# Performance work log

Measured on AMD Instinct MI355X. Metric: run time of the kernel, lower is better.

Reference implementation:

```python
import jax, jax.numpy as jnp
import numpy as np
import math


def _alibi_slopes(h):
    # h must be a power of 2 here (h=16); matches pow2slopes in the source
    start = 2.0 ** (-2.0 ** (-(math.log2(h) - 3.0)))
    return jnp.asarray([start ** (i + 1) for i in range(h)], dtype=jnp.float32)


def setup_inputs() -> dict:
    key = jax.random.key(0)
    ks = jax.random.split(key, 7)
    B, N, d, h, r = 2, 2048, 1024, 16, 32
    dk = d // h
    x = jax.random.normal(ks[0], (B, N, d), dtype=jnp.float32)
    # causal additive mask (standard usage of the optional `mask` arg)
    i = jnp.arange(N)[:, None]
    j = jnp.arange(N)[None, :]
    mask = jnp.where(j > i, jnp.float32(-1e9), jnp.float32(0.0))[None, None]  # [1,1,N,N]
    s = 1.0 / math.sqrt(d)
    Wq = jax.random.normal(ks[1], (d, d), dtype=jnp.float32) * s
    Wk = jax.random.normal(ks[2], (d, d), dtype=jnp.float32) * s
    Wv = jax.random.normal(ks[3], (d, d), dtype=jnp.float32) * s
    # orthogonal init of U, as in nn.init.orthogonal_
    U, _ = jnp.linalg.qr(jax.random.normal(ks[4], (dk, r), dtype=jnp.float32))
    Wproj = jax.random.normal(ks[5], (d, h * r), dtype=jnp.float32) * (1.0 / math.sqrt(h * r))
    return {"x": x, "mask": mask, "Wq": Wq, "Wk": Wk, "Wv": Wv, "U": U,
            "Wproj": Wproj, "rel_bias_tokens": N}


def reference(x, mask, Wq, Wk, Wv, U, Wproj, rel_bias_tokens):
    B, N, d = x.shape
    dk, r = U.shape
    h = d // dk

    def lowrank_proj(W):
        # Linear(d,d,bias=False) then per-head low-rank projection by U
        y = (x @ W.T).reshape(B, N, h, dk)          # [B,N,h,dk]
        return jnp.einsum('bnhk,kr->bhnr', y, U)     # [B,h,N,r]

    q = lowrank_proj(Wq)
    k = lowrank_proj(Wk)
    v = lowrank_proj(Wv)

    # scores scaled by sqrt(dk) (NOT sqrt(r)) -- faithful to source
    att = jnp.einsum('bhnr,bhmr->bhnm', q, k) / math.sqrt(dk)  # [B,h,N,N]

    # q_len == k_len branch: alibi bias + mask
    i = jnp.arange(rel_bias_tokens)[:, None]
    j = jnp.arange(rel_bias_tokens)[None, :]
    dist = jnp.maximum(j - i, 0).astype(att.dtype)             # clamp_min(0)
    slopes = _alibi_slopes(h)
    att = att + (-slopes[:, None, None] * dist)[None] + mask

    z = jnp.einsum('bhnm,bhmr->bhnr', jax.nn.softmax(att, axis=-1), v)
    z = z.transpose(0, 2, 1, 3).reshape(B, N, h * r)
    # dropout is identity in eval
    return z @ Wproj.T
```

## Files before the change

kernel.cpp:

```cpp
#include <hip/hip_runtime.h>
#include <hip/hip_bf16.h>
#include <stdint.h>

typedef unsigned short u16;
typedef __attribute__((ext_vector_type(4))) short short4v;
typedef __attribute__((ext_vector_type(8))) short short8;
typedef __attribute__((ext_vector_type(4))) float f32x4;

#define NB 2
#define NN 2048
#define ND 1024
#define NH 16
#define NR 32
#define NM (NB*NN)
#define NHR 512
#define NQKV 1536

static __device__ __forceinline__ u16 f2bf(float f) {
  union { float f; uint32_t u; } v; v.f = f;
  uint32_t r = v.u + 0x7fffu + ((v.u >> 16) & 1u);
  return (u16)(r >> 16);
}
static __device__ __forceinline__ u16 fastbf(float f) {
  union { float f; uint32_t u; } v; v.f = f;
  return (u16)((v.u + 0x8000u) >> 16);
}

typedef __attribute__((address_space(1))) unsigned int as1_u32;
typedef __attribute__((address_space(3))) unsigned int as3_u32;

static __device__ __forceinline__ void async_copy16(void* lds, const void* g) {
  __builtin_amdgcn_global_load_lds((as1_u32*)(uintptr_t)g,
                                   (as3_u32*)(uint32_t)(uintptr_t)lds,
                                   16, 0, 0);
}

__global__ void cast_f32_bf16(const float* __restrict__ in, u16* __restrict__ o,
                              int n8) {
  int i = blockIdx.x * 256 + threadIdx.x;
  if (i >= n8) return;
  const float4* p = (const float4*)in + (size_t)i * 2;
  float4 a = p[0], b = p[1];
  short8 v;
  v[0] = f2bf(a.x); v[1] = f2bf(a.y); v[2] = f2bf(a.z); v[3] = f2bf(a.w);
  v[4] = f2bf(b.x); v[5] = f2bf(b.y); v[6] = f2bf(b.z); v[7] = f2bf(b.w);
  *((short8*)o + i) = v;
}

__global__ __launch_bounds__(256, 2)
void build_wct(const float* __restrict__ Wq, const float* __restrict__ Wk,
               const float* __restrict__ Wv, const float* __restrict__ U,
               u16* __restrict__ WcT) {
  __shared__ float sU[64 * 32];
  const int tid = threadIdx.x;
  #pragma unroll
  for (int t = 0; t < 2; ++t)
    ((float4*)sU)[t * 256 + tid] = ((const float4*)U)[t * 256 + tid];
  __syncthreads();
  const int wh = blockIdx.y;
  const int w = wh >> 4, head = wh & 15;
  const float* W = (w == 0) ? Wq : (w == 1 ? Wk : Wv);
  const int i = blockIdx.x * 256 + tid;
  const float* Wcol = W + (size_t)head * 64 * ND + i;
  float acc[32];
  #pragma unroll
  for (int rr = 0; rr < 32; ++rr) acc[rr] = 0.f;
  for (int kk = 0; kk < 64; ++kk) {
    const float wv = Wcol[(size_t)kk * ND];
    const float4* u4 = (const float4*)&sU[kk * 32];
    #pragma unroll
    for (int r4 = 0; r4 < 8; ++r4) {
      float4 u = u4[r4];
      acc[r4 * 4 + 0] += wv * u.x;
      acc[r4 * 4 + 1] += wv * u.y;
      acc[r4 * 4 + 2] += wv * u.z;
      acc[r4 * 4 + 3] += wv * u.w;
    }
  }
  const float sc = (w == 0) ? 0.125f : 1.0f;
  const int colBase = w * 512 + head * 32;
  #pragma unroll
  for (int rr = 0; rr < 32; ++rr)
    WcT[(size_t)(colBase + rr) * ND + i] = f2bf(acc[rr] * sc);
}

template<int EPI>
__global__ __launch_bounds__(256, 2)
void gemm_bt(const u16* __restrict__ A, int lda,
             const u16* __restrict__ BT, int ldb, int K,
             u16* __restrict__ o0, u16* __restrict__ o1, u16* __restrict__ o2,
             float* __restrict__ fo) {
  __shared__ __align__(16) u16 lA[128 * 64];
  __shared__ __align__(16) u16 lB[128 * 64];
  const int tid = threadIdx.x;
  const int lane = tid & 63, quad = lane >> 4, l16 = lane & 15;
  const int wave = tid >> 6;
  const int wm = (wave >> 1) * 64, wn = (wave & 1) * 64;
  const int rowBase = blockIdx.y * 128, colBase = blockIdx.x * 128;

  f32x4 acc[4][4];
  #pragma unroll
  for (int i = 0; i < 4; ++i)
    #pragma unroll
    for (int j = 0; j < 4; ++j)
      acc[i][j] = (f32x4){0.f, 0.f, 0.f, 0.f};

  for (int kt = 0; kt < K; kt += 64) {
    #pragma unroll
    for (int it = 0; it < 4; ++it) {
      const int cid = it * 256 + tid;
      const int row = cid >> 3, pc = cid & 7;
      const int gc = pc ^ (row & 7);
      async_copy16(&lA[cid * 8], &A[(size_t)(rowBase + row) * lda + kt + gc * 8]);
      async_copy16(&lB[cid * 8], &BT[(size_t)(colBase + row) * ldb + kt + gc * 8]);
    }
    __syncthreads();
    #pragma unroll
    for (int ks = 0; ks < 64; ks += 32) {
      short8 fa[4], fb[4];
      #pragma unroll
      for (int t = 0; t < 4; ++t) {
        const int ra = wm + t * 16 + l16;
        const int pa = ((ks >> 3) + quad) ^ (ra & 7);
        fa[t] = *(const short8*)&lA[ra * 64 + pa * 8];
        const int rb = wn + t * 16 + l16;
        const int pb = ((ks >> 3) + quad) ^ (rb & 7);
        fb[t] = *(const short8*)&lB[rb * 64 + pb * 8];
      }
      #pragma unroll
      for (int mt = 0; mt < 4; ++mt)
        #pragma unroll
        for (int nt = 0; nt < 4; ++nt)
          acc[mt][nt] = __builtin_amdgcn_mfma_f32_16x16x32_bf16(
              fa[mt], fb[nt], acc[mt][nt], 0, 0, 0);
    }
    __syncthreads();
  }

  #pragma unroll
  for (int mt = 0; mt < 4; ++mt) {
    const int gr0 = rowBase + wm + mt * 16 + quad * 4;
    #pragma unroll
    for (int nt = 0; nt < 4; ++nt) {
      const int c = colBase + wn + nt * 16 + l16;
      #pragma unroll
      for (int j = 0; j < 4; ++j) {
        const float v = acc[mt][nt][j];
        const int row = gr0 + j;
        if (EPI == 0) {
          fo[(size_t)row * 1024 + c] = v;
        } else {
          const int b = row >> 11, n = row & (NN - 1);
          const int w = c >> 9, ch = c & 511, head = ch >> 5, rr = ch & 31;
          if (w == 0)
            o0[(size_t)(((b * NH + head) * NN + n)) * NR + rr] = f2bf(v);
          else if (w == 1)
            o1[(size_t)(((b * NH + head) * NN + n)) * NR + rr] = f2bf(v);
          else
            o2[(size_t)((b * NH + head) * NR + rr) * NN + n] = f2bf(v);
        }
      }
    }
  }
}

__global__ __launch_bounds__(256, 4)
void flash_attn(const u16* __restrict__ q, const u16* __restrict__ k,
                const u16* __restrict__ vt, u16* __restrict__ z) {
  __shared__ __align__(16) u16 lK[2][64 * 32];
  __shared__ __align__(16) u16 lV[2][32 * 64];
  const int bh = blockIdx.y;
  const int b = bh >> 4, head = bh & 15;
  const int tid = threadIdx.x;
  const int lane = tid & 63, quad = lane >> 4, l16 = lane & 15;
  const int wave = tid >> 6;
  const int qblk = gridDim.x - 1 - blockIdx.x;
  const int qb0 = qblk * 64;
  const int qbase = qb0 + wave * 16;
  const int qq = qbase + l16;

  const u16* qp = q  + (size_t)bh * NN * NR;
  const u16* kp = k  + (size_t)bh * NN * NR;
  const u16* vp = vt + (size_t)bh * NR * NN;

  const short8 bq = *(const short8*)&qp[(size_t)(qbase + l16) * NR + quad * 8];

  f32x4 Ot0 = (f32x4){0.f,0.f,0.f,0.f};
  f32x4 Ot1 = (f32x4){0.f,0.f,0.f,0.f};
  float ls = 0.f;

  const int krow = tid >> 2, kc = tid & 3;
  const int vrow = tid >> 3, vpc = tid & 7;
  const int vgc = vpc ^ (vrow & 7);

  #define STAGE(kt_, buf_) do {                                            \
    const int m0_ = (kt_) * 64;                                            \
    async_copy16(&lK[buf_][tid * 8], &kp[(size_t)(m0_ + krow) * NR + kc * 8]); \
    async_copy16(&lV[buf_][tid * 8], &vp[(size_t)vrow * NN + m0_ + vgc * 8]);  \
  } while (0)

  STAGE(0, 0);
  int buf = 0;
  for (int kt = 0; kt <= qblk; ++kt) {
    asm volatile("s_waitcnt vmcnt(0) lgkmcnt(0)" ::: "memory");
    __syncthreads();
    if (kt < qblk) STAGE(kt + 1, buf ^ 1);

    const int m0 = kt * 64;
    f32x4 s[4];
    const f32x4 zero = (f32x4){0.f,0.f,0.f,0.f};
    #pragma unroll
    for (int g = 0; g < 4; ++g) {
      const short8 ak = *(const short8*)&lK[buf][(16 * g + l16) * 32 + quad * 8];
      s[g] = __builtin_amdgcn_mfma_f32_16x16x32_bf16(ak, bq, zero, 0, 0, 0);
    }
    if (kt == qblk) {
      #pragma unroll
      for (int g = 0; g < 4; ++g)
        #pragma unroll
        for (int j = 0; j < 4; ++j)
          if (m0 + 16 * g + quad * 4 + j > qq) s[g][j] = -1e30f;
    }
    #pragma unroll
    for (int g = 0; g < 4; ++g) {
      const float p0 = __expf(s[g][0]), p1 = __expf(s[g][1]);
      const float p2 = __expf(s[g][2]), p3 = __expf(s[g][3]);
      ls += (p0 + p1) + (p2 + p3);
      short4v bp;
      bp[0] = fastbf(p0); bp[1] = fastbf(p1); bp[2] = fastbf(p2); bp[3] = fastbf(p3);
      const int c0 = 2 * g + (quad >> 1), off = (quad & 1) * 4;
      const short4v av0 = *(const short4v*)
          &lV[buf][l16 * 64 + ((c0 ^ (l16 & 7)) * 8) + off];
      const short4v av1 = *(const short4v*)
          &lV[buf][(16 + l16) * 64 + ((c0 ^ ((16 + l16) & 7)) * 8) + off];
      Ot0 = __builtin_amdgcn_mfma_f32_16x16x16bf16_1k(av0, bp, Ot0, 0, 0, 0);
      Ot1 = __builtin_amdgcn_mfma_f32_16x16x16bf16_1k(av1, bp, Ot1, 0, 0, 0);
    }
    asm volatile("s_waitcnt lgkmcnt(0)" ::: "memory");
    __syncthreads();
    buf ^= 1;
  }
  #undef STAGE

  ls += __shfl_xor(ls, 16);
  ls += __shfl_xor(ls, 32);
  const float inv = 1.f / ls;

  short4v o0, o1;
  #pragma unroll
  for (int j = 0; j < 4; ++j) {
    o0[j] = f2bf(Ot0[j] * inv);
    o1[j] = f2bf(Ot1[j] * inv);
  }
  u16* zr = z + (size_t)(b * NN + qq) * NHR + head * NR;
  *(short4v*)&zr[quad * 4]      = o0;
  *(short4v*)&zr[16 + quad * 4] = o1;
}

extern "C" void kernel_launch(void* const* d_in, const int* in_sizes, int n_in,
                              void* d_out, int out_size, void* d_ws, size_t ws_size,
                              hipStream_t stream) {
  const float* x     = (const float*)d_in[0];
  const float* Wq    = (const float*)d_in[2];
  const float* Wk    = (const float*)d_in[3];
  const float* Wv    = (const float*)d_in[4];
  const float* U     = (const float*)d_in[5];
  const float* Wproj = (const float*)d_in[6];
  float* out = (float*)d_out;

  u16* ws  = (u16*)d_ws;
  u16* xb  = ws;
  u16* z   = ws;
  u16* Wpb = ws + (size_t)4 * 1024 * 1024;
  u16* WcT = Wpb + (size_t)512 * 1024;
  u16* q   = ws + (size_t)6 * 1024 * 1024;
  u16* kk  = q  + (size_t)NB * NH * NN * NR;
  u16* vt  = kk + (size_t)NB * NH * NN * NR;

  cast_f32_bf16<<<(NM * ND / 8 + 255) / 256, 256, 0, stream>>>(x, xb, NM * ND / 8);
  cast_f32_bf16<<<(ND * NHR / 8 + 255) / 256, 256, 0, stream>>>(Wproj, Wpb, ND * NHR / 8);
  build_wct<<<dim3(ND / 256, 48), 256, 0, stream>>>(Wq, Wk, Wv, U, WcT);
  gemm_bt<1><<<dim3(NQKV / 128, NM / 128), 256, 0, stream>>>(
      xb, ND, WcT, ND, ND, q, kk, vt, nullptr);
  flash_attn<<<dim3(NN / 64, NB * NH), 256, 0, stream>>>(q, kk, vt, z);
  gemm_bt<0><<<dim3(ND / 128, NM / 128), 256, 0, stream>>>(
      z, NHR, Wpb, NHR, NHR, nullptr, nullptr, nullptr, out);
}
```

Measured before the change: 183.6 us.

## Merge prep kernels, add XCD-aware GEMM block swizzle, raise attention occupancy

Three launches (two fp32→bf16 casts and the fused W·U weight build) become one prep kernel that picks its role from the block index, removing two launch gaps. The GEMM now maps flat block ids so each XCD gets a contiguous band of rows, which should improve L2 reuse of the A tiles. The flash attention launch bound goes from 4 to 6 blocks per CU, which may force register spills. The swizzle assumes the grid row count is 32 (NM/128) across 8 XCDs.

```diff
diff --git a/kernel.cpp b/kernel.cpp
--- a/kernel.cpp
+++ b/kernel.cpp
@@ -35,53 +35,56 @@
                                    16, 0, 0);
 }
 
-__global__ void cast_f32_bf16(const float* __restrict__ in, u16* __restrict__ o,
-                              int n8) {
-  int i = blockIdx.x * 256 + threadIdx.x;
-  if (i >= n8) return;
-  const float4* p = (const float4*)in + (size_t)i * 2;
-  float4 a = p[0], b = p[1];
-  short8 v;
-  v[0] = f2bf(a.x); v[1] = f2bf(a.y); v[2] = f2bf(a.z); v[3] = f2bf(a.w);
-  v[4] = f2bf(b.x); v[5] = f2bf(b.y); v[6] = f2bf(b.z); v[7] = f2bf(b.w);
-  *((short8*)o + i) = v;
-}
-
 __global__ __launch_bounds__(256, 2)
-void build_wct(const float* __restrict__ Wq, const float* __restrict__ Wk,
-               const float* __restrict__ Wv, const float* __restrict__ U,
-               u16* __restrict__ WcT) {
+void prep(const float* __restrict__ x, const float* __restrict__ Wproj,
+          const float* __restrict__ Wq, const float* __restrict__ Wk,
+          const float* __restrict__ Wv, const float* __restrict__ U,
+          u16* __restrict__ xb, u16* __restrict__ Wpb, u16* __restrict__ WcT) {
   __shared__ float sU[64 * 32];
+  const int blk = blockIdx.x;
   const int tid = threadIdx.x;
-  #pragma unroll
-  for (int t = 0; t < 2; ++t)
-    ((float4*)sU)[t * 256 + tid] = ((const float4*)U)[t * 256 + tid];
-  __syncthreads();
-  const int wh = blockIdx.y;
-  const int w = wh >> 4, head = wh & 15;
-  const float* W = (w == 0) ? Wq : (w == 1 ? Wk : Wv);
-  const int i = blockIdx.x * 256 + tid;
-  const float* Wcol = W + (size_t)head * 64 * ND + i;
-  float acc[32];
-  #pragma unroll
-  for (int rr = 0; rr < 32; ++rr) acc[rr] = 0.f;
-  for (int kk = 0; kk < 64; ++kk) {
-    const float wv = Wcol[(size_t)kk * ND];
-    const float4* u4 = (const float4*)&sU[kk * 32];
-    #pragma unroll
-    for (int r4 = 0; r4 < 8; ++r4) {
-      float4 u = u4[r4];
-      acc[r4 * 4 + 0] += wv * u.x;
-      acc[r4 * 4 + 1] += wv * u.y;
-      acc[r4 * 4 + 2] += wv * u.z;
-      acc[r4 * 4 + 3] += wv * u.w;
-    }
-  }
-  const float sc = (w == 0) ? 0.125f : 1.0f;
-  const int colBase = w * 512 + head * 32;
-  #pragma unroll
-  for (int rr = 0; rr < 32; ++rr)
-    WcT[(size_t)(colBase + rr) * ND + i] = f2bf(acc[rr] * sc);
+  if (blk < 2304) {
+    const float* in = (blk < 2048) ? x : Wproj;
+    u16* o = (blk < 2048) ? xb : Wpb;
+    const int i = ((blk < 2048) ? blk : (blk - 2048)) * 256 + tid;
+    const float4* p = (const float4*)in + (size_t)i * 2;
+    float4 a = p[0], b2 = p[1];
+    short8 v;
+    v[0] = f2bf(a.x);  v[1] = f2bf(a.y);  v[2] = f2bf(a.z);  v[3] = f2bf(a.w);
+    v[4] = f2bf(b2.x); v[5] = f2bf(b2.y); v[6] = f2bf(b2.z); v[7] = f2bf(b2.w);
+    *((short8*)o + i) = v;
+  } else {
+    #pragma unroll
+    for (int t = 0; t < 2; ++t)
+      ((float4*)sU)[t * 256 + tid] = ((const float4*)U)[t * 256 + tid];
+    __syncthreads();
+    const int local = blk - 2304;
+    const int wh = local >> 2;
+    const int w = wh >> 4, head = wh & 15;
+    const float* W = (w == 0) ? Wq : (w == 1 ? Wk : Wv);
+    const int i = (local & 3) * 256 + tid;
+    const float* Wcol = W + (size_t)head * 64 * ND + i;
+    float acc[32];
+    #pragma unroll
+    for (int rr = 0; rr < 32; ++rr) acc[rr] = 0.f;
+    for (int kk = 0; kk < 64; ++kk) {
+      const float wv = Wcol[(size_t)kk * ND];
+      const float4* u4 = (const float4*)&sU[kk * 32];
+      #pragma unroll
+      for (int r4 = 0; r4 < 8; ++r4) {
+        float4 u = u4[r4];
+        acc[r4 * 4 + 0] += wv * u.x;
+        acc[r4 * 4 + 1] += wv * u.y;
+        acc[r4 * 4 + 2] += wv * u.z;
+        acc[r4 * 4 + 3] += wv * u.w;
+      }
+    }
+    const float sc = (w == 0) ? 0.125f : 1.0f;
+    const int colBase = w * 512 + head * 32;
+    #pragma unroll
+    for (int rr = 0; rr < 32; ++rr)
+      WcT[(size_t)(colBase + rr) * ND + i] = f2bf(acc[rr] * sc);
+  }
 }
 
 template<int EPI>
@@ -96,7 +99,11 @@
   const int lane = tid & 63, quad = lane >> 4, l16 = lane & 15;
   const int wave = tid >> 6;
   const int wm = (wave >> 1) * 64, wn = (wave & 1) * 64;
-  const int rowBase = blockIdx.y * 128, colBase = blockIdx.x * 128;
+  const int GX = gridDim.x;
+  const int flat = blockIdx.y * GX + blockIdx.x;
+  const int xcd = flat & 7, s = flat >> 3;
+  const int brow = xcd * 4 + s / GX, bcol = s % GX;
+  const int rowBase = brow * 128, colBase = bcol * 128;
 
   f32x4 acc[4][4];
   #pragma unroll
@@ -164,7 +171,7 @@
   }
 }
 
-__global__ __launch_bounds__(256, 4)
+__global__ __launch_bounds__(256, 6)
 void flash_attn(const u16* __restrict__ q, const u16* __restrict__ k,
                 const u16* __restrict__ vt, u16* __restrict__ z) {
   __shared__ __align__(16) u16 lK[2][64 * 32];
@@ -277,9 +284,7 @@
   u16* kk  = q  + (size_t)NB * NH * NN * NR;
   u16* vt  = kk + (size_t)NB * NH * NN * NR;
 
-  cast_f32_bf16<<<(NM * ND / 8 + 255) / 256, 256, 0, stream>>>(x, xb, NM * ND / 8);
-  cast_f32_bf16<<<(ND * NHR / 8 + 255) / 256, 256, 0, stream>>>(Wproj, Wpb, ND * NHR / 8);
-  build_wct<<<dim3(ND / 256, 48), 256, 0, stream>>>(Wq, Wk, Wv, U, WcT);
+  prep<<<2496, 256, 0, stream>>>(x, Wproj, Wq, Wk, Wv, U, xb, Wpb, WcT);
   gemm_bt<1><<<dim3(NQKV / 128, NM / 128), 256, 0, stream>>>(
       xb, ND, WcT, ND, ND, q, kk, vt, nullptr);
   flash_attn<<<dim3(NN / 64, NB * NH), 256, 0, stream>>>(q, kk, vt, z);
```

Result: no change. 180.5 us (-1.7%).
